# Kernel optimization log

Measured on AMD Instinct MI355X. Metric: run time of the kernel, lower is better.

## Reference

```python
import jax, jax.numpy as jnp
import numpy as np

Z_DIM = 128
K = 64
RANK = 16
B = 65536


def setup_inputs() -> dict:
    key = jax.random.key(0)
    k1, k2, k3 = jax.random.split(key, 3)
    z = jax.random.normal(k1, (B, Z_DIM), dtype=jnp.float32)
    # nn.Linear(z_dim, K*rank): weight [K*rank, z_dim], bias [K*rank]
    bound = 1.0 / np.sqrt(Z_DIM)
    W = jax.random.uniform(k2, (K * RANK, Z_DIM), dtype=jnp.float32, minval=-bound, maxval=bound)
    b = jax.random.uniform(k3, (K * RANK,), dtype=jnp.float32, minval=-bound, maxval=bound)
    return {"z": z, "W": W, "b": b}


def reference(z, W, b):
    bsz = z.shape[0]
    # linear projection: [B, K*rank]
    w = z @ W.T + b
    w = w.reshape(bsz, K, RANK) + 1e-6
    # batched reduced QR on small K x rank matrices (fp32, like torch .float())
    q, _ = jnp.linalg.qr(w.astype(jnp.float32), mode="reduced")
    return q.astype(z.dtype)
```

## Files before the change

kernel.cpp:

```cpp
#include <hip/hip_runtime.h>

#define TOTAL_B 65536
#define NKR 1024
#define ZD 128

__global__ __launch_bounds__(256) void gemm_zwt(
    const float* __restrict__ z, const float* __restrict__ W,
    const float* __restrict__ bias, float* __restrict__ out)
{
    __shared__ float zs[32][132];
    __shared__ float ws[32][132];

    const int tid = threadIdx.x;
    const int tx = tid & 15;
    const int ty = tid >> 4;
    const int m0 = blockIdx.y * 128;
    const int n0 = blockIdx.x * 128;

    float acc[8][8];
    #pragma unroll
    for (int i = 0; i < 8; ++i)
        #pragma unroll
        for (int j = 0; j < 8; ++j) acc[i][j] = 0.f;

    const int kq = (tid & 7) * 4;
    const int mr = tid >> 3;

    for (int kc = 0; kc < ZD; kc += 32) {
        #pragma unroll
        for (int p = 0; p < 4; ++p) {
            int ml = mr + p * 32;
            float4 v = *(const float4*)(z + (size_t)(m0 + ml) * ZD + kc + kq);
            zs[kq + 0][ml] = v.x; zs[kq + 1][ml] = v.y;
            zs[kq + 2][ml] = v.z; zs[kq + 3][ml] = v.w;
            float4 u = *(const float4*)(W + (size_t)(n0 + ml) * ZD + kc + kq);
            ws[kq + 0][ml] = u.x; ws[kq + 1][ml] = u.y;
            ws[kq + 2][ml] = u.z; ws[kq + 3][ml] = u.w;
        }
        __syncthreads();
        #pragma unroll 8
        for (int k = 0; k < 32; ++k) {
            float4 a0 = *(const float4*)&zs[k][ty * 8];
            float4 a1 = *(const float4*)&zs[k][ty * 8 + 4];
            float4 c0 = *(const float4*)&ws[k][tx * 8];
            float4 c1 = *(const float4*)&ws[k][tx * 8 + 4];
            float zr[8] = {a0.x, a0.y, a0.z, a0.w, a1.x, a1.y, a1.z, a1.w};
            float wr[8] = {c0.x, c0.y, c0.z, c0.w, c1.x, c1.y, c1.z, c1.w};
            #pragma unroll
            for (int i = 0; i < 8; ++i)
                #pragma unroll
                for (int j = 0; j < 8; ++j)
                    acc[i][j] = fmaf(zr[i], wr[j], acc[i][j]);
        }
        __syncthreads();
    }

    float bv[8];
    #pragma unroll
    for (int j = 0; j < 8; ++j) bv[j] = bias[n0 + tx * 8 + j] + 1e-6f;

    #pragma unroll
    for (int i = 0; i < 8; ++i) {
        size_t base = (size_t)(m0 + ty * 8 + i) * NKR + n0 + tx * 8;
        float4 o0, o1;
        o0.x = acc[i][0] + bv[0]; o0.y = acc[i][1] + bv[1];
        o0.z = acc[i][2] + bv[2]; o0.w = acc[i][3] + bv[3];
        o1.x = acc[i][4] + bv[4]; o1.y = acc[i][5] + bv[5];
        o1.z = acc[i][6] + bv[6]; o1.w = acc[i][7] + bv[7];
        *(float4*)(out + base) = o0;
        *(float4*)(out + base + 4) = o1;
    }
}

template <int CTRL>
__device__ __forceinline__ float dpp_add(float v) {
    int x = __builtin_amdgcn_update_dpp(0, __float_as_int(v), CTRL, 0xF, 0xF, false);
    return v + __int_as_float(x);
}

__device__ __forceinline__ float rsum16(float v) {
    v = dpp_add<0x128>(v);
    v = dpp_add<0x124>(v);
    v = dpp_add<0x122>(v);
    v = dpp_add<0x121>(v);
    return v;
}

__global__ __launch_bounds__(256) void qr_batched(float* __restrict__ buf)
{
    const int tid = threadIdx.x;
    const int lq = tid & 15;
    const int item = (blockIdx.x * 256 + tid) >> 4;

    float* p = buf + (size_t)item * NKR + lq * 16;

    float a[16][4];
    #pragma unroll
    for (int i = 0; i < 4; ++i) {
        #pragma unroll
        for (int cc = 0; cc < 16; cc += 4) {
            float4 v = *(const float4*)(p + i * 256 + cc);
            a[cc + 0][i] = v.x; a[cc + 1][i] = v.y;
            a[cc + 2][i] = v.z; a[cc + 3][i] = v.w;
        }
    }

    float tau[16];

    #pragma unroll
    for (int j = 0; j < 16; ++j) {
        float x0 = a[j][0], x1 = a[j][1], x2 = a[j][2], x3 = a[j][3];
        float x0m = (lq > j) ? x0 : 0.f;
        float pp = fmaf(x0m, x0m, fmaf(x1, x1, fmaf(x2, x2, x3 * x3)));
        float xn2   = rsum16(pp);
        float alpha = rsum16((lq == j) ? x0 : 0.f);

        float rr   = sqrtf(fmaf(alpha, alpha, xn2));
        float beta = (alpha >= 0.f) ? -rr : rr;
        float tj   = (beta - alpha) / beta;
        float sc   = 1.f / (alpha - beta);
        if (xn2 == 0.f) { tj = 0.f; sc = 0.f; }
        tau[j] = tj;

        float v0 = (lq == j) ? 1.f : ((lq > j) ? x0 * sc : 0.f);
        float v1 = x1 * sc, v2 = x2 * sc, v3 = x3 * sc;
        a[j][0] = v0; a[j][1] = v1; a[j][2] = v2; a[j][3] = v3;

        #pragma unroll
        for (int c = j + 1; c < 16; ++c) {
            float d = rsum16(fmaf(v0, a[c][0],
                        fmaf(v1, a[c][1],
                        fmaf(v2, a[c][2], v3 * a[c][3]))));
            float t = -tj * d;
            a[c][0] = fmaf(t, v0, a[c][0]);
            a[c][1] = fmaf(t, v1, a[c][1]);
            a[c][2] = fmaf(t, v2, a[c][2]);
            a[c][3] = fmaf(t, v3, a[c][3]);
        }
    }

    #pragma unroll 1
    for (int c0 = 0; c0 < 16; c0 += 4) {
        float qq[4][4];
        #pragma unroll
        for (int k = 0; k < 4; ++k) {
            qq[k][0] = (lq == c0 + k) ? 1.f : 0.f;
            qq[k][1] = 0.f; qq[k][2] = 0.f; qq[k][3] = 0.f;
        }
        #pragma unroll
        for (int j = 15; j >= 0; --j) {
            if (j <= c0 + 3) {
                float tj = tau[j];
                #pragma unroll
                for (int k = 0; k < 4; ++k) {
                    float d = rsum16(fmaf(a[j][0], qq[k][0],
                                fmaf(a[j][1], qq[k][1],
                                fmaf(a[j][2], qq[k][2], a[j][3] * qq[k][3]))));
                    float t = (j <= c0 + k) ? (-tj * d) : 0.f;
                    qq[k][0] = fmaf(t, a[j][0], qq[k][0]);
                    qq[k][1] = fmaf(t, a[j][1], qq[k][1]);
                    qq[k][2] = fmaf(t, a[j][2], qq[k][2]);
                    qq[k][3] = fmaf(t, a[j][3], qq[k][3]);
                }
            }
        }
        #pragma unroll
        for (int i = 0; i < 4; ++i) {
            float4 vv = {qq[0][i], qq[1][i], qq[2][i], qq[3][i]};
            *(float4*)(p + i * 256 + c0) = vv;
        }
    }
}

extern "C" void kernel_launch(void* const* d_in, const int* in_sizes, int n_in,
                              void* d_out, int out_size, void* d_ws, size_t ws_size,
                              hipStream_t stream) {
    const float* z = (const float*)d_in[0];
    const float* W = (const float*)d_in[1];
    const float* b = (const float*)d_in[2];
    float* out = (float*)d_out;

    dim3 ggrid(NKR / 128, TOTAL_B / 128);
    hipLaunchKernelGGL(gemm_zwt, ggrid, dim3(256), 0, stream, z, W, b, out);
    hipLaunchKernelGGL(qr_batched, dim3(TOTAL_B / 16), dim3(256), 0, stream, out);
}
```

Baseline: 685.6 us.

## Prefetch GEMM tiles, conflict-free LDS reads, fast rcp/sqrt, in-place Q accumulation

```diff
diff --git a/kernel.cpp b/kernel.cpp
--- a/kernel.cpp
+++ b/kernel.cpp
@@ -26,24 +26,42 @@
     const int kq = (tid & 7) * 4;
     const int mr = tid >> 3;
 
+    const float* gz = z + (size_t)(m0 + mr) * ZD + kq;
+    const float* gw = W + (size_t)(n0 + mr) * ZD + kq;
+
+    float4 vz[4], vw[4];
+    #pragma unroll
+    for (int p = 0; p < 4; ++p) {
+        vz[p] = *(const float4*)(gz + (size_t)p * 32 * ZD);
+        vw[p] = *(const float4*)(gw + (size_t)p * 32 * ZD);
+    }
+
+    #pragma unroll
     for (int kc = 0; kc < ZD; kc += 32) {
         #pragma unroll
         for (int p = 0; p < 4; ++p) {
             int ml = mr + p * 32;
-            float4 v = *(const float4*)(z + (size_t)(m0 + ml) * ZD + kc + kq);
-            zs[kq + 0][ml] = v.x; zs[kq + 1][ml] = v.y;
-            zs[kq + 2][ml] = v.z; zs[kq + 3][ml] = v.w;
-            float4 u = *(const float4*)(W + (size_t)(n0 + ml) * ZD + kc + kq);
-            ws[kq + 0][ml] = u.x; ws[kq + 1][ml] = u.y;
-            ws[kq + 2][ml] = u.z; ws[kq + 3][ml] = u.w;
+            zs[kq + 0][ml] = vz[p].x; zs[kq + 1][ml] = vz[p].y;
+            zs[kq + 2][ml] = vz[p].z; zs[kq + 3][ml] = vz[p].w;
+            ws[kq + 0][ml] = vw[p].x; ws[kq + 1][ml] = vw[p].y;
+            ws[kq + 2][ml] = vw[p].z; ws[kq + 3][ml] = vw[p].w;
         }
         __syncthreads();
+
+        if (kc + 32 < ZD) {
+            #pragma unroll
+            for (int p = 0; p < 4; ++p) {
+                vz[p] = *(const float4*)(gz + (size_t)p * 32 * ZD + kc + 32);
+                vw[p] = *(const float4*)(gw + (size_t)p * 32 * ZD + kc + 32);
+            }
+        }
+
         #pragma unroll 8
         for (int k = 0; k < 32; ++k) {
-            float4 a0 = *(const float4*)&zs[k][ty * 8];
-            float4 a1 = *(const float4*)&zs[k][ty * 8 + 4];
-            float4 c0 = *(const float4*)&ws[k][tx * 8];
-            float4 c1 = *(const float4*)&ws[k][tx * 8 + 4];
+            float4 a0 = *(const float4*)&zs[k][ty * 4];
+            float4 a1 = *(const float4*)&zs[k][64 + ty * 4];
+            float4 c0 = *(const float4*)&ws[k][tx * 4];
+            float4 c1 = *(const float4*)&ws[k][64 + tx * 4];
             float zr[8] = {a0.x, a0.y, a0.z, a0.w, a1.x, a1.y, a1.z, a1.w};
             float wr[8] = {c0.x, c0.y, c0.z, c0.w, c1.x, c1.y, c1.z, c1.w};
             #pragma unroll
@@ -55,20 +73,24 @@
         __syncthreads();
     }
 
-    float bv[8];
-    #pragma unroll
-    for (int j = 0; j < 8; ++j) bv[j] = bias[n0 + tx * 8 + j] + 1e-6f;
+    float bv0[4], bv1[4];
+    #pragma unroll
+    for (int j = 0; j < 4; ++j) {
+        bv0[j] = bias[n0 + tx * 4 + j] + 1e-6f;
+        bv1[j] = bias[n0 + 64 + tx * 4 + j] + 1e-6f;
+    }
 
     #pragma unroll
     for (int i = 0; i < 8; ++i) {
-        size_t base = (size_t)(m0 + ty * 8 + i) * NKR + n0 + tx * 8;
+        int row = (i < 4) ? (ty * 4 + i) : (64 + ty * 4 + i - 4);
+        size_t base = (size_t)(m0 + row) * NKR + n0;
         float4 o0, o1;
-        o0.x = acc[i][0] + bv[0]; o0.y = acc[i][1] + bv[1];
-        o0.z = acc[i][2] + bv[2]; o0.w = acc[i][3] + bv[3];
-        o1.x = acc[i][4] + bv[4]; o1.y = acc[i][5] + bv[5];
-        o1.z = acc[i][6] + bv[6]; o1.w = acc[i][7] + bv[7];
-        *(float4*)(out + base) = o0;
-        *(float4*)(out + base + 4) = o1;
+        o0.x = acc[i][0] + bv0[0]; o0.y = acc[i][1] + bv0[1];
+        o0.z = acc[i][2] + bv0[2]; o0.w = acc[i][3] + bv0[3];
+        o1.x = acc[i][4] + bv1[0]; o1.y = acc[i][5] + bv1[1];
+        o1.z = acc[i][6] + bv1[2]; o1.w = acc[i][7] + bv1[3];
+        *(float4*)(out + base + tx * 4) = o0;
+        *(float4*)(out + base + 64 + tx * 4) = o1;
     }
 }
 
@@ -115,10 +137,11 @@
         float xn2   = rsum16(pp);
         float alpha = rsum16((lq == j) ? x0 : 0.f);
 
-        float rr   = sqrtf(fmaf(alpha, alpha, xn2));
+        float rr   = __builtin_amdgcn_sqrtf(fmaf(alpha, alpha, xn2));
         float beta = (alpha >= 0.f) ? -rr : rr;
-        float tj   = (beta - alpha) / beta;
-        float sc   = 1.f / (alpha - beta);
+        float dba  = beta - alpha;
+        float tj   = dba * __builtin_amdgcn_rcpf(beta);
+        float sc   = -__builtin_amdgcn_rcpf(dba);
         if (xn2 == 0.f) { tj = 0.f; sc = 0.f; }
         tau[j] = tj;
 
@@ -139,35 +162,34 @@
         }
     }
 
-    #pragma unroll 1
-    for (int c0 = 0; c0 < 16; c0 += 4) {
-        float qq[4][4];
-        #pragma unroll
-        for (int k = 0; k < 4; ++k) {
-            qq[k][0] = (lq == c0 + k) ? 1.f : 0.f;
-            qq[k][1] = 0.f; qq[k][2] = 0.f; qq[k][3] = 0.f;
-        }
-        #pragma unroll
-        for (int j = 15; j >= 0; --j) {
-            if (j <= c0 + 3) {
-                float tj = tau[j];
-                #pragma unroll
-                for (int k = 0; k < 4; ++k) {
-                    float d = rsum16(fmaf(a[j][0], qq[k][0],
-                                fmaf(a[j][1], qq[k][1],
-                                fmaf(a[j][2], qq[k][2], a[j][3] * qq[k][3]))));
-                    float t = (j <= c0 + k) ? (-tj * d) : 0.f;
-                    qq[k][0] = fmaf(t, a[j][0], qq[k][0]);
-                    qq[k][1] = fmaf(t, a[j][1], qq[k][1]);
-                    qq[k][2] = fmaf(t, a[j][2], qq[k][2]);
-                    qq[k][3] = fmaf(t, a[j][3], qq[k][3]);
-                }
-            }
-        }
-        #pragma unroll
-        for (int i = 0; i < 4; ++i) {
-            float4 vv = {qq[0][i], qq[1][i], qq[2][i], qq[3][i]};
-            *(float4*)(p + i * 256 + c0) = vv;
+    #pragma unroll
+    for (int j = 15; j >= 0; --j) {
+        float tj = tau[j];
+        float v0 = a[j][0], v1 = a[j][1], v2 = a[j][2], v3 = a[j][3];
+        #pragma unroll
+        for (int c = j + 1; c < 16; ++c) {
+            float d = rsum16(fmaf(v0, a[c][0],
+                        fmaf(v1, a[c][1],
+                        fmaf(v2, a[c][2], v3 * a[c][3]))));
+            float t = -tj * d;
+            a[c][0] = fmaf(t, v0, a[c][0]);
+            a[c][1] = fmaf(t, v1, a[c][1]);
+            a[c][2] = fmaf(t, v2, a[c][2]);
+            a[c][3] = fmaf(t, v3, a[c][3]);
+        }
+        float nt = -tj;
+        a[j][0] = fmaf(nt, v0, (lq == j) ? 1.f : 0.f);
+        a[j][1] = nt * v1;
+        a[j][2] = nt * v2;
+        a[j][3] = nt * v3;
+    }
+
+    #pragma unroll
+    for (int i = 0; i < 4; ++i) {
+        #pragma unroll
+        for (int cc = 0; cc < 16; cc += 4) {
+            float4 vv = {a[cc + 0][i], a[cc + 1][i], a[cc + 2][i], a[cc + 3][i]};
+            *(float4*)(p + i * 256 + cc) = vv;
         }
     }
 }
```

Result: faster. 605.1 us (-11.7%).
